# Kernel optimization log

Measured on AMD Instinct MI355X. Metric: run time of the kernel, lower is better.

## Reference

```python
import jax, jax.numpy as jnp
import numpy as np
import math


def setup_inputs() -> dict:
    key = jax.random.key(0)
    ks = jax.random.split(key, 10)
    b, n, d, h = 2, 1024, 1024, 16
    hd = d // h
    std = 0.02
    x = jax.random.normal(ks[0], (b, n, d), jnp.float32)
    Wq = jax.random.normal(ks[1], (d, d), jnp.float32) * std
    Wk = jax.random.normal(ks[2], (d, d), jnp.float32) * std
    Wv = jax.random.normal(ks[3], (d, d), jnp.float32) * std
    Wo = jax.random.normal(ks[4], (d, d), jnp.float32) * std
    Ww1 = jax.random.normal(ks[5], (d, hd), jnp.float32) * std
    Ww2 = jax.random.normal(ks[6], (hd, d), jnp.float32) * std
    Wb = jax.random.normal(ks[7], (d, h), jnp.float32) * std
    Wf = jax.random.normal(ks[8], (d, h), jnp.float32) * std
    # delta initialized so sigmoid(delta) = threshold = 0.99
    delta = jnp.full((h,), math.log(0.99 / (1.0 - 0.99)), jnp.float32)
    return dict(x=x, Wq=Wq, Wk=Wk, Wv=Wv, Wo=Wo, Ww1=Ww1, Ww2=Ww2, Wb=Wb, Wf=Wf, delta=delta)


def reference(x, Wq, Wk, Wv, Wo, Ww1, Ww2, Wb, Wf, delta):
    b, n, d = x.shape
    h = delta.shape[0]
    hd = d // h
    scale = hd ** -0.5
    q = (x @ Wq).reshape(b, n, h, hd)
    k = (x @ Wk).reshape(b, n, h, hd)
    v = (x @ Wv).reshape(b, n, h, hd)
    w = ((x @ Ww1) @ Ww2).reshape(b, n, h, hd)
    # l2-normalize write directions per head
    w = w * jax.lax.rsqrt(jnp.sum(w * w, axis=-1, keepdims=True) + 1e-6)
    beta = 2.0 * jax.nn.sigmoid(x @ Wb)                      # (b,n,h)
    log_f = jax.nn.log_sigmoid((x @ Wf + delta).astype(jnp.float32))  # (b,n,h)
    bt = jnp.transpose(beta, (0, 2, 1))                      # (b,h,n)
    # PaTH attention: logit_{t,j} = q_t^T H_t H_{t-1} ... H_{j+1} k_j, H_s = I - beta_s w_s w_s^T.
    # UT transform: c_{s,j} = w_s . k_j^{(s-1)} satisfies (I + L) C = tril(W K^T, -1)
    # with L_{s,r} = beta_r (w_s . w_r) for r < s.
    A = jnp.einsum('bshd,brhd->bhsr', w, w)                  # w_s . w_r
    L = jnp.tril(A, -1) * bt[:, :, None, :]                  # (b,h,n,n), strictly lower
    Mlow = jnp.tril(jnp.einsum('bshd,bjhd->bhsj', w, k), -1)
    C = jax.scipy.linalg.solve_triangular(L, Mlow, lower=True, unit_diagonal=True)
    # transformed score: S_{t,j} = q_t.k_j - sum_{j<s<=t} beta_s (q_t.w_s) c_{s,j}
    G = jnp.tril(jnp.einsum('bthd,bshd->bhts', q, w) * bt[:, :, None, :])
    S = jnp.einsum('bthd,bjhd->bhtj', q, k) - G @ C          # (b,h,n,n)
    # forgetting-gate decay: add F_t - F_j (cumulative log-sigmoid gates)
    Fc = jnp.cumsum(jnp.transpose(log_f, (0, 2, 1)), axis=-1)  # (b,h,n)
    logits = S * scale + Fc[..., :, None] - Fc[..., None, :]
    mask = jnp.tril(jnp.ones((n, n), bool))
    logits = jnp.where(mask, logits, -jnp.inf)
    P = jax.nn.softmax(logits, axis=-1)
    o = jnp.einsum('bhtj,bjhd->bthd', P, v).reshape(b, n, d)
    return o @ Wo
```

## Files before the change

### kernel.cpp

```cpp
#include <hip/hip_runtime.h>
#include <hip/hip_bf16.h>

#define DEV static __device__ __forceinline__

constexpr float SM_SCALE = 0.125f;

typedef __attribute__((ext_vector_type(8))) short s16x8;
typedef __attribute__((ext_vector_type(8))) unsigned short u16x8;
typedef __attribute__((ext_vector_type(4))) unsigned short u16x4;
typedef __attribute__((ext_vector_type(4))) float f32x4;

DEV float bf2f(unsigned short u) {
  union { unsigned int i; float f; } v; v.i = ((unsigned int)u) << 16; return v.f;
}
DEV unsigned short f2bf(float f) {
  union { float f; unsigned int i; } v; v.f = f;
  unsigned int r = v.i + 0x7fffu + ((v.i >> 16) & 1u);
  return (unsigned short)(r >> 16);
}
DEV void tri_unrank(int r, int& k, int& i) {
  k = (int)((sqrtf(8.f * r + 1.f) - 1.f) * 0.5f);
  while (k * (k + 1) / 2 > r) --k;
  while ((k + 1) * (k + 2) / 2 <= r) ++k;
  i = r - k * (k + 1) / 2;
}
DEV void glds16(const void* g, void* l) {
  __builtin_amdgcn_global_load_lds(
      (const __attribute__((address_space(1))) void*)g,
      (__attribute__((address_space(3))) void*)l, 16, 0, 0);
}

constexpr size_t OFF_XB   = 0;
constexpr size_t OFF_WQT  = 4194304;
constexpr size_t OFF_BL   = 4194304;
constexpr size_t OFF_WKT  = 6291456;
constexpr size_t OFF_BFT  = 6291456;
constexpr size_t OFF_WVT  = 8388608;
constexpr size_t OFF_WOT  = 10485760;
constexpr size_t OFF_W1T  = 12582912;
constexpr size_t OFF_W2T  = 12713984;
constexpr size_t OFF_Q16  = 12845056;
constexpr size_t OFF_K16  = 17039360;
constexpr size_t OFF_VT   = 21233664;
constexpr size_t OFF_WN16 = 25427968;
constexpr size_t OFF_WB16 = 29622272;
constexpr size_t OFF_WNF  = 33816576;
constexpr size_t OFF_OB   = 33816576;
constexpr size_t OFF_WPRE = 38010880;
constexpr size_t OFF_FC   = 38273024;
constexpr size_t OFF_L    = 38404096;
constexpr size_t OFF_CT   = 105512960;
constexpr size_t OFF_G    = 172621824;
constexpr size_t OFF_MR   = 239730688;
constexpr size_t OFF_LR   = 239861760;
constexpr size_t OFF_UI   = 239992832;
constexpr size_t OFF_U128 = 244187136;

__global__ __launch_bounds__(256) void prep_all(
    const float* __restrict__ W0, const float* __restrict__ W1,
    const float* __restrict__ W2, const float* __restrict__ W3,
    const float* __restrict__ Ww1, const float* __restrict__ Ww2,
    const float* __restrict__ x,
    unsigned short* __restrict__ D0, unsigned short* __restrict__ D1,
    unsigned short* __restrict__ D2, unsigned short* __restrict__ D3,
    unsigned short* __restrict__ D4, unsigned short* __restrict__ D5,
    unsigned short* __restrict__ xb) {
  int bidx = blockIdx.x;
  int t = threadIdx.x;
  if (bidx >= 1536) {
    int i = ((bidx - 1536) * 256 + t) * 8;
    float4 a = *(const float4*)(x + i);
    float4 b = *(const float4*)(x + i + 4);
    u16x8 o;
    o[0] = f2bf(a.x); o[1] = f2bf(a.y); o[2] = f2bf(a.z); o[3] = f2bf(a.w);
    o[4] = f2bf(b.x); o[5] = f2bf(b.y); o[6] = f2bf(b.z); o[7] = f2bf(b.w);
    *(u16x8*)(xb + i) = o;
    return;
  }
  int z = bidx >> 8, xy = bidx & 255;
  int bx = xy & 15, by = xy >> 4;
  const float* src; unsigned short* dst; int R, C;
  if (z == 0) { src = W0; dst = D0; R = 1024; C = 1024; }
  else if (z == 1) { src = W1; dst = D1; R = 1024; C = 1024; }
  else if (z == 2) { src = W2; dst = D2; R = 1024; C = 1024; }
  else if (z == 3) { src = W3; dst = D3; R = 1024; C = 1024; }
  else if (z == 4) { src = Ww1; dst = D4; R = 1024; C = 64; }
  else { src = Ww2; dst = D5; R = 64; C = 1024; }
  int c0 = bx * 64, r0 = by * 64;
  if (c0 >= C || r0 >= R) return;
  __shared__ float tile[64 * 65];
#pragma unroll
  for (int i = 0; i < 16; ++i) {
    int lin = t + i * 256; int r = lin >> 6, c = lin & 63;
    tile[r * 65 + c] = src[(size_t)(r0 + r) * C + c0 + c];
  }
  __syncthreads();
#pragma unroll
  for (int i = 0; i < 16; ++i) {
    int lin = t + i * 256; int c = lin >> 6, r = lin & 63;
    dst[(size_t)(c0 + c) * R + r0 + r] = f2bf(tile[r * 65 + c]);
  }
}

__global__ __launch_bounds__(256) void bfprep(const float* __restrict__ Wb,
    const float* __restrict__ Wf, unsigned short* __restrict__ BFT) {
  int idx = blockIdx.x * 256 + threadIdx.x;
  int j = idx >> 10, i = idx & 1023;
  float v = 0.f;
  if (j < 16) v = Wb[i * 16 + j];
  else if (j < 32) v = Wf[i * 16 + (j - 16)];
  BFT[idx] = f2bf(v);
}

__global__ __launch_bounds__(256) void bgfc(const float* __restrict__ BL,
    const float* __restrict__ delta, float* __restrict__ Beta, float* __restrict__ Fc) {
  int bh = blockIdx.x;
  int b = bh >> 4, h = bh & 15;
  int t = threadIdx.x;
  __shared__ float buf[1024];
  __shared__ float tsum[256];
  float dh = delta[h];
#pragma unroll
  for (int i = 0; i < 4; ++i) {
    int n = t + i * 256;
    int row = (b << 10) + n;
    float braw = BL[row * 64 + h];
    Beta[row * 16 + h] = 2.f / (1.f + __expf(-braw));
    float lraw = BL[row * 64 + 16 + h] + dh;
    buf[n] = (lraw >= 0.f) ? -log1pf(__expf(-lraw)) : (lraw - log1pf(__expf(lraw)));
  }
  __syncthreads();
  float loc[4]; float run = 0.f;
#pragma unroll
  for (int i = 0; i < 4; ++i) { run += buf[t * 4 + i]; loc[i] = run; }
  tsum[t] = run;
  __syncthreads();
  for (int off = 1; off < 256; off <<= 1) {
    float add = (t >= off) ? tsum[t - off] : 0.f;
    __syncthreads();
    tsum[t] += add;
    __syncthreads();
  }
  float excl = tsum[t] - run;
#pragma unroll
  for (int i = 0; i < 4; ++i) Fc[bh * 1024 + t * 4 + i] = excl + loc[i];
}

__global__ __launch_bounds__(256) void proj_big(const unsigned short* __restrict__ xb,
    const unsigned short* __restrict__ WqT, const unsigned short* __restrict__ WkT,
    const unsigned short* __restrict__ WvT, unsigned short* __restrict__ Q16,
    unsigned short* __restrict__ K16, unsigned short* __restrict__ VT) {
  int idx = blockIdx.x;
  const unsigned short *A, *BT; unsigned short* out; int m0, n0;
  if (idx < 256) {
    int my = idx >> 4, nx = idx & 15;
    m0 = my * 128; A = xb;
    if (nx < 8) { BT = WqT; out = Q16; n0 = nx * 128; }
    else { BT = WkT; out = K16; n0 = (nx - 8) * 128; }
  } else {
    int r = idx - 256; int bz = r >> 6; int rem = r & 63;
    m0 = (rem >> 3) * 128; n0 = (rem & 7) * 128;
    A = WvT; BT = xb + ((size_t)bz << 20); out = VT + ((size_t)bz << 20);
  }
  int t = threadIdx.x;
  int w = t >> 6, l = t & 63;
  int wr = w >> 1, wc = w & 1;
  int fr = l & 15, fq = l >> 4;
  __shared__ unsigned short As[128 * 64];
  __shared__ unsigned short Bs[128 * 64];
  f32x4 acc[4][4];
#pragma unroll
  for (int m = 0; m < 4; ++m)
#pragma unroll
    for (int c = 0; c < 4; ++c) acc[m][c] = (f32x4){0.f, 0.f, 0.f, 0.f};
  for (int k0 = 0; k0 < 1024; k0 += 64) {
    __syncthreads();
#pragma unroll
    for (int i = 0; i < 4; ++i) {
      int cid = t + i * 256;
      int row = cid >> 3, ch = cid & 7;
      int chs = ch ^ (row & 7);
      glds16(A + (size_t)(m0 + row) * 1024 + k0 + chs * 8, (char*)As + cid * 16);
      glds16(BT + (size_t)(n0 + row) * 1024 + k0 + chs * 8, (char*)Bs + cid * 16);
    }
    __syncthreads();
#pragma unroll
    for (int kh = 0; kh < 2; ++kh) {
      s16x8 af[4], bfv[4];
#pragma unroll
      for (int m = 0; m < 4; ++m) {
        int ra = wr * 64 + 16 * m + fr;
        af[m] = *(const s16x8*)((char*)As + (((ra << 7) + (kh << 6) + (fq << 4)) ^ ((ra & 7) << 4)));
      }
#pragma unroll
      for (int c = 0; c < 4; ++c) {
        int rb = wc * 64 + 16 * c + fr;
        bfv[c] = *(const s16x8*)((char*)Bs + (((rb << 7) + (kh << 6) + (fq << 4)) ^ ((rb & 7) << 4)));
      }
#pragma unroll
      for (int m = 0; m < 4; ++m)
#pragma unroll
        for (int c = 0; c < 4; ++c)
          acc[m][c] = __builtin_amdgcn_mfma_f32_16x16x32_bf16(af[m], bfv[c], acc[m][c], 0, 0, 0);
    }
  }
#pragma unroll
  for (int m = 0; m < 4; ++m) {
#pragma unroll
    for (int c = 0; c < 4; ++c) {
      int col = n0 + wc * 64 + 16 * c + fr;
#pragma unroll
      for (int r = 0; r < 4; ++r) {
        int grow = m0 + wr * 64 + 16 * m + fq * 4 + r;
        out[(size_t)grow * 1024 + col] = f2bf(acc[m][c][r]);
      }
    }
  }
}

__global__ __launch_bounds__(256) void proj_small(const unsigned short* __restrict__ A,
    const unsigned short* __restrict__ W1T, const unsigned short* __restrict__ BFT,
    unsigned short* __restrict__ Wpre, float* __restrict__ BL) {
  int nt = blockIdx.x;
  const unsigned short* BT = nt ? BFT : W1T;
  __shared__ unsigned short As[64 * 64];
  __shared__ unsigned short Bs[64 * 64];
  int m0 = blockIdx.y * 64;
  int t = threadIdx.x;
  int w = t >> 6, l = t & 63, fr = l & 15;
  int koB = (l >> 4) * 16;
  f32x4 acc[4];
#pragma unroll
  for (int c = 0; c < 4; ++c) acc[c] = (f32x4){0.f, 0.f, 0.f, 0.f};
  for (int k0 = 0; k0 < 1024; k0 += 64) {
    __syncthreads();
#pragma unroll
    for (int i = 0; i < 2; ++i) {
      int cid = t + i * 256;
      int row = cid >> 3, ch = cid & 7;
      int chs = ch ^ (row & 7);
      glds16(A + (size_t)(m0 + row) * 1024 + k0 + chs * 8, (char*)As + cid * 16);
      glds16(BT + (size_t)row * 1024 + k0 + chs * 8, (char*)Bs + cid * 16);
    }
    __syncthreads();
#pragma unroll
    for (int kh = 0; kh < 2; ++kh) {
      int ra = 16 * w + fr;
      s16x8 a = *(const s16x8*)((char*)As + (((ra << 7) + (kh << 6) + koB) ^ ((ra & 7) << 4)));
#pragma unroll
      for (int c = 0; c < 4; ++c) {
        int rb = 16 * c + fr;
        s16x8 bb = *(const s16x8*)((char*)Bs + (((rb << 7) + (kh << 6) + koB) ^ ((rb & 7) << 4)));
        acc[c] = __builtin_amdgcn_mfma_f32_16x16x32_bf16(a, bb, acc[c], 0, 0, 0);
      }
    }
  }
  int rbase = m0 + 16 * w + ((l >> 4) << 2);
#pragma unroll
  for (int c = 0; c < 4; ++c) {
    int col = 16 * c + fr;
#pragma unroll
    for (int r = 0; r < 4; ++r) {
      if (nt) BL[(size_t)(rbase + r) * 64 + col] = acc[c][r];
      else Wpre[(size_t)(rbase + r) * 64 + col] = f2bf(acc[c][r]);
    }
  }
}

template<int F32OUT>
__global__ __launch_bounds__(256) void gemm_nt(const unsigned short* __restrict__ A,
    const unsigned short* __restrict__ BT, void* __restrict__ out,
    int M, int N, int K) {
  __shared__ unsigned short As[64 * 64];
  __shared__ unsigned short Bs[64 * 64];
  int m0 = blockIdx.y * 64, n0 = blockIdx.x * 64;
  int t = threadIdx.x;
  int w = t >> 6, l = t & 63, fr = l & 15;
  int koB = (l >> 4) * 16;
  f32x4 acc[4];
#pragma unroll
  for (int c = 0; c < 4; ++c) acc[c] = (f32x4){0.f, 0.f, 0.f, 0.f};
  for (int k0 = 0; k0 < K; k0 += 64) {
    __syncthreads();
#pragma unroll
    for (int i = 0; i < 2; ++i) {
      int cid = t + i * 256;
      int row = cid >> 3, ch = cid & 7;
      int chs = ch ^ (row & 7);
      glds16(A + (size_t)(m0 + row) * K + k0 + chs * 8, (char*)As + cid * 16);
      glds16(BT + (size_t)(n0 + row) * K + k0 + chs * 8, (char*)Bs + cid * 16);
    }
    __syncthreads();
#pragma unroll
    for (int kh = 0; kh < 2; ++kh) {
      int ra = 16 * w + fr;
      s16x8 a = *(const s16x8*)((char*)As + (((ra << 7) + (kh << 6) + koB) ^ ((ra & 7) << 4)));
#pragma unroll
      for (int c = 0; c < 4; ++c) {
        int rb = 16 * c + fr;
        s16x8 bb = *(const s16x8*)((char*)Bs + (((rb << 7) + (kh << 6) + koB) ^ ((rb & 7) << 4)));
        acc[c] = __builtin_amdgcn_mfma_f32_16x16x32_bf16(a, bb, acc[c], 0, 0, 0);
      }
    }
  }
  int rbase = m0 + 16 * w + ((l >> 4) << 2);
#pragma unroll
  for (int c = 0; c < 4; ++c) {
    int col = n0 + 16 * c + fr;
#pragma unroll
    for (int r = 0; r < 4; ++r) {
      if (F32OUT) ((float*)out)[(size_t)(rbase + r) * N + col] = acc[c][r];
      else ((unsigned short*)out)[(size_t)(rbase + r) * N + col] = f2bf(acc[c][r]);
    }
  }
}

__global__ __launch_bounds__(256) void wnorm2(const unsigned short* __restrict__ WNF,
    const float* __restrict__ Beta, unsigned short* __restrict__ WN,
    unsigned short* __restrict__ WB) {
  int row = blockIdx.x;
  int wave = threadIdx.x >> 6, lane = threadIdx.x & 63;
#pragma unroll
  for (int i = 0; i < 4; ++i) {
    int hh = wave * 4 + i;
    size_t idx = ((size_t)row << 10) + hh * 64 + lane;
    float v = bf2f(WNF[idx]);
    float ss = v * v;
#pragma unroll
    for (int off = 1; off < 64; off <<= 1) ss += __shfl_xor(ss, off);
    float wn = v * rsqrtf(ss + 1e-6f);
    WN[idx] = f2bf(wn);
    WB[idx] = f2bf(wn * Beta[row * 16 + hh]);
  }
}

__global__ __launch_bounds__(256) void pairLG(const unsigned short* __restrict__ WN,
    const unsigned short* __restrict__ Q, const unsigned short* __restrict__ WB,
    unsigned short* __restrict__ Lg, unsigned short* __restrict__ Gg) {
  int idx = blockIdx.x;
  int bh = idx & 31, r0r = idx >> 5;
  int tb2, jb2; tri_unrank(r0r, tb2, jb2);
  int b = bh >> 4, h = bh & 15;
  int m0 = tb2 * 128, n0 = jb2 * 128;
  int t = threadIdx.x;
  int w = t >> 6, l = t & 63;
  int wr = w >> 1, wc = w & 1;
  int fr = l & 15, fq = l >> 4;
// ... 176 lines not shown
  }
}

__global__ __launch_bounds__(256) void u128build(const unsigned short* __restrict__ Lb,
    const unsigned short* __restrict__ UI, unsigned short* __restrict__ U128) {
  int ib = blockIdx.x, bh = blockIdx.y;
  int t = threadIdx.x, w = t >> 6, l = t & 63, fr = l & 15, fq = l >> 4;
  int s0 = ib * 128;
  size_t base = (size_t)bh << 20;
  const unsigned short* Ua = UI + (((size_t)(bh * 16 + 2 * ib)) << 12);
  const unsigned short* Uc = UI + (((size_t)(bh * 16 + 2 * ib + 1)) << 12);
  unsigned short* Uo = U128 + (((size_t)(bh * 8 + ib)) << 14);
  __shared__ unsigned short UaT[64 * 64];
  __shared__ unsigned short T1T[64 * 64];
#pragma unroll
  for (int i = 0; i < 2; ++i) {
    int cid = t + i * 256;
    int s = cid >> 3, ch = cid & 7;
    u16x8 v = *(const u16x8*)(Ua + s * 64 + ch * 8);
#pragma unroll
    for (int e = 0; e < 8; ++e) {
      int j = ch * 8 + e;
      int byt = ((j << 7) + (s << 1)) ^ ((j & 7) << 4);
      *(unsigned short*)((char*)UaT + byt) = v[e];
    }
  }
#pragma unroll
  for (int i = 0; i < 8; ++i) {
    int cid = t + i * 256;
    int row = cid >> 4, ch = cid & 15;
    if (row < 64) {
      if (ch < 8) *(u16x8*)(Uo + row * 128 + ch * 8) = *(const u16x8*)(Ua + row * 64 + ch * 8);
      else { u16x8 z = {0,0,0,0,0,0,0,0}; *(u16x8*)(Uo + row * 128 + ch * 8) = z; }
    } else if (ch >= 8) {
      *(u16x8*)(Uo + row * 128 + ch * 8) = *(const u16x8*)(Uc + (row - 64) * 64 + (ch - 8) * 8);
    }
  }
  __syncthreads();
  f32x4 a1[4];
#pragma unroll
  for (int c = 0; c < 4; ++c) a1[c] = (f32x4){0.f, 0.f, 0.f, 0.f};
#pragma unroll
  for (int kc = 0; kc < 2; ++kc) {
    s16x8 af = *(const s16x8*)(Lb + base + ((size_t)(s0 + 64 + 16 * w + fr) << 10) + s0 + kc * 32 + fq * 8);
#pragma unroll
    for (int c = 0; c < 4; ++c) {
      int j = 16 * c + fr;
      s16x8 bb = *(const s16x8*)((char*)UaT + (((j << 7) + (kc << 6) + (fq << 4)) ^ ((j & 7) << 4)));
      a1[c] = __builtin_amdgcn_mfma_f32_16x16x32_bf16(af, bb, a1[c], 0, 0, 0);
    }
  }
#pragma unroll
  for (int c = 0; c < 4; ++c) {
    int gj = 16 * c + fr;
    int sb = 16 * w + fq * 4;
    u16x4 pk;
#pragma unroll
    for (int r = 0; r < 4; ++r) pk[r] = f2bf(a1[c][r]);
    *(u16x4*)((char*)T1T + (((gj << 7) + (sb << 1)) ^ ((gj & 7) << 4))) = pk;
  }
  __syncthreads();
  f32x4 a2[4];
#pragma unroll
  for (int c = 0; c < 4; ++c) a2[c] = (f32x4){0.f, 0.f, 0.f, 0.f};
#pragma unroll
  for (int kc = 0; kc < 2; ++kc) {
    s16x8 af = *(const s16x8*)(Uc + (16 * w + fr) * 64 + kc * 32 + fq * 8);
#pragma unroll
    for (int c = 0; c < 4; ++c) {
      int j = 16 * c + fr;
      s16x8 bb = *(const s16x8*)((char*)T1T + (((j << 7) + (kc << 6) + (fq << 4)) ^ ((j & 7) << 4)));
      a2[c] = __builtin_amdgcn_mfma_f32_16x16x32_bf16(af, bb, a2[c], 0, 0, 0);
    }
  }
#pragma unroll
  for (int c = 0; c < 4; ++c) {
    int gj = 16 * c + fr;
#pragma unroll
    for (int r = 0; r < 4; ++r)
      Uo[(64 + 16 * w + fq * 4 + r) * 128 + gj] = f2bf(a2[c][r]);
  }
}

__global__ __launch_bounds__(256) void solve128(const unsigned short* __restrict__ WN,
    const unsigned short* __restrict__ Kk, const unsigned short* __restrict__ Lb,
    const unsigned short* __restrict__ U128, unsigned short* __restrict__ CT, int ib) {
  int jb = blockIdx.x, bh = blockIdx.y;
  int b = bh >> 4, h = bh & 15;
  int t = threadIdx.x, w = t >> 6, l = t & 63;
  int wr = w >> 1, wc = w & 1, fr = l & 15, fq = l >> 4;
  int s0 = ib * 128, j0 = jb * 128;
  size_t base = (size_t)bh << 20;
  __shared__ unsigned short sh[128 * 128];
  unsigned short* As = sh;
  unsigned short* Bs = sh + 128 * 64;
  unsigned short* rT = sh;
  const unsigned short* Wb_ = WN + ((size_t)b << 20) + h * 64;
  const unsigned short* Kb_ = Kk + ((size_t)b << 20) + h * 64;

  f32x4 acc[4][4];
#pragma unroll
  for (int m = 0; m < 4; ++m)
#pragma unroll
    for (int c = 0; c < 4; ++c) acc[m][c] = (f32x4){0.f, 0.f, 0.f, 0.f};
  int nst = (jb == ib) ? 1 : 1 + 2 * (ib - jb);
  for (int st = 0; st < nst; ++st) {
    __syncthreads();
#pragma unroll
    for (int i = 0; i < 4; ++i) {
      int cid = t + i * 256;
      int row = cid >> 3, ch = cid & 7;
      int chs = ch ^ (row & 7);
      const unsigned short *ga, *gb;
      if (st == 0) {
        ga = Wb_ + ((size_t)(s0 + row) << 10) + chs * 8;
        gb = Kb_ + ((size_t)(j0 + row) << 10) + chs * 8;
      } else {
        int rb = 2 * jb + st - 1;
        ga = Lb + base + ((size_t)(s0 + row) << 10) + rb * 64 + chs * 8;
        gb = CT + base + ((size_t)(j0 + row) << 10) + rb * 64 + chs * 8;
      }
      glds16(ga, (char*)As + cid * 16);
      glds16(gb, (char*)Bs + cid * 16);
    }
    __syncthreads();
#pragma unroll
    for (int kh = 0; kh < 2; ++kh) {
      s16x8 af[4], bfv[4];
#pragma unroll
      for (int m = 0; m < 4; ++m) {
        int ra = wr * 64 + 16 * m + fr;
        af[m] = *(const s16x8*)((char*)As + (((ra << 7) + (kh << 6) + (fq << 4)) ^ ((ra & 7) << 4)));
      }
#pragma unroll
      for (int c = 0; c < 4; ++c) {
        int rb2 = wc * 64 + 16 * c + fr;
        bfv[c] = *(const s16x8*)((char*)Bs + (((rb2 << 7) + (kh << 6) + (fq << 4)) ^ ((rb2 & 7) << 4)));
      }
#pragma unroll
      for (int m = 0; m < 4; ++m)
#pragma unroll
        for (int c = 0; c < 4; ++c)
          acc[m][c] = __builtin_amdgcn_mfma_f32_16x16x32_bf16(af[m], bfv[c], acc[m][c], 0, 0, 0);
    }
  }
  __syncthreads();
#pragma unroll
  for (int m = 0; m < 4; ++m) {
#pragma unroll
    for (int c = 0; c < 4; ++c) {
      int jl = wc * 64 + 16 * c + fr;
      int sb = wr * 64 + 16 * m + fq * 4;
      u16x4 pk;
#pragma unroll
      for (int r = 0; r < 4; ++r) {
        float v = acc[m][c][r];
        if (jb == ib && jl >= sb + r) v = 0.f;
        pk[r] = f2bf(v);
      }
      int byt = ((jl << 8) + (sb << 1)) ^ ((jl & 15) << 4);
      *(u16x4*)((char*)rT + byt) = pk;
    }
  }
  __syncthreads();
  const unsigned short* U = U128 + (((size_t)(bh * 8 + ib)) << 14);
  f32x4 a2[4][4];
#pragma unroll
  for (int m = 0; m < 4; ++m)
#pragma unroll
    for (int c = 0; c < 4; ++c) a2[m][c] = (f32x4){0.f, 0.f, 0.f, 0.f};
#pragma unroll
  for (int kc = 0; kc < 4; ++kc) {
    s16x8 uf[4], bfv[4];
#pragma unroll
    for (int m = 0; m < 4; ++m)
      uf[m] = *(const s16x8*)(U + (wr * 64 + 16 * m + fr) * 128 + kc * 32 + fq * 8);
#pragma unroll
    for (int c = 0; c < 4; ++c) {
      int jl = wc * 64 + 16 * c + fr;
      bfv[c] = *(const s16x8*)((char*)rT + (((jl << 8) + (kc << 6) + (fq << 4)) ^ ((jl & 15) << 4)));
    }
#pragma unroll
    for (int m = 0; m < 4; ++m)
#pragma unroll
      for (int c = 0; c < 4; ++c)
        a2[m][c] = __builtin_amdgcn_mfma_f32_16x16x32_bf16(uf[m], bfv[c], a2[m][c], 0, 0, 0);
  }
#pragma unroll
  for (int m = 0; m < 4; ++m) {
#pragma unroll
    for (int c = 0; c < 4; ++c) {
      int gj = wc * 64 + 16 * c + fr;
      int sb = wr * 64 + 16 * m + fq * 4;
      u16x4 pk;
#pragma unroll
      for (int r = 0; r < 4; ++r) pk[r] = f2bf(a2[m][c][r]);
      *(u16x4*)(CT + base + ((size_t)(j0 + gj) << 10) + s0 + sb) = pk;
    }
  }
}

__global__ __launch_bounds__(256) void rowstat(const unsigned short* __restrict__ S,
    const float* __restrict__ Fc, float* __restrict__ MR, float* __restrict__ LR) {
  int bh = blockIdx.y;
  int t = blockIdx.x * 4 + (threadIdx.x >> 6);
  int l = threadIdx.x & 63;
  size_t base = (size_t)bh << 20;
  const unsigned short* srow = S + base + ((size_t)t << 10);
  float vals[16]; float vmax = -1e30f;
#pragma unroll
  for (int i = 0; i < 2; ++i) {
    int c0 = i * 512 + l * 8;
    u16x8 sv = *(const u16x8*)(srow + c0);
    float4 f0 = *(const float4*)(Fc + bh * 1024 + c0);
    float4 f1 = *(const float4*)(Fc + bh * 1024 + c0 + 4);
#pragma unroll
    for (int e = 0; e < 8; ++e) {
      float fc = e < 4 ? ((const float*)&f0)[e] : ((const float*)&f1)[e - 4];
      float v = (c0 + e <= t) ? bf2f(sv[e]) * SM_SCALE - fc : -1e30f;
      vals[i * 8 + e] = v; vmax = fmaxf(vmax, v);
    }
  }
#pragma unroll
  for (int o = 1; o < 64; o <<= 1) vmax = fmaxf(vmax, __shfl_xor(vmax, o));
  float sum = 0.f;
#pragma unroll
  for (int e = 0; e < 16; ++e) sum += __expf(vals[e] - vmax);
#pragma unroll
  for (int o = 1; o < 64; o <<= 1) sum += __shfl_xor(sum, o);
  if (l == 0) { MR[bh * 1024 + t] = vmax; LR[bh * 1024 + t] = sum; }
}

__global__ __launch_bounds__(256) void pv_kernel(const unsigned short* __restrict__ S,
    const unsigned short* __restrict__ VT, const float* __restrict__ Fc,
    const float* __restrict__ MR, const float* __restrict__ LR,
    unsigned short* __restrict__ Ob) {
  int idx = blockIdx.x;
  int bh = idx & 31, rank = idx >> 5;
  int tb = 15 - rank;
  int b = bh >> 4, h = bh & 15;
  int t0 = tb * 64;
  int t = threadIdx.x, w = t >> 6, l = t & 63, fr = l & 15, fq = l >> 4;
  __shared__ unsigned short Pl[64 * 64];
  size_t base = (size_t)bh << 20;
  f32x4 acc[4];
#pragma unroll
  for (int c = 0; c < 4; ++c) acc[c] = (f32x4){0.f,0.f,0.f,0.f};
  for (int jb = 0; jb <= tb; ++jb) {
    int j0 = jb * 64;
    __syncthreads();
#pragma unroll
    for (int i = 0; i < 2; ++i) {
      int cid = t + i * 256;
      int row = cid >> 3, ch = cid & 7;
      int grow = t0 + row;
      u16x8 sv = *(const u16x8*)(S + base + ((size_t)grow << 10) + j0 + ch * 8);
      float4 f0 = *(const float4*)(Fc + bh * 1024 + j0 + ch * 8);
      float4 f1 = *(const float4*)(Fc + bh * 1024 + j0 + ch * 8 + 4);
      float m = MR[bh * 1024 + grow];
      u16x8 pv;
#pragma unroll
      for (int e = 0; e < 8; ++e) {
        float fc = e < 4 ? ((const float*)&f0)[e] : ((const float*)&f1)[e - 4];
        float p = __expf(bf2f(sv[e]) * SM_SCALE - fc - m);
        if (jb == tb && ch * 8 + e > row) p = 0.f;
        pv[e] = f2bf(p);
      }
      int byt = ((row << 7) + (ch << 4)) ^ ((row & 7) << 4);
      *(u16x8*)((char*)Pl + byt) = pv;
    }
    __syncthreads();
#pragma unroll
    for (int kh = 0; kh < 2; ++kh) {
      int ra = 16 * w + fr;
      s16x8 a = *(const s16x8*)((char*)Pl + (((ra << 7) + (kh << 6) + (fq << 4)) ^ ((ra & 7) << 4)));
#pragma unroll
      for (int c = 0; c < 4; ++c) {
        s16x8 bb = *(const s16x8*)(VT + ((size_t)bh * 64 + 16 * c + fr) * 1024 + j0 + kh * 32 + fq * 8);
        acc[c] = __builtin_amdgcn_mfma_f32_16x16x32_bf16(a, bb, acc[c], 0, 0, 0);
      }
    }
  }
  float inv[4];
#pragma unroll
  for (int r = 0; r < 4; ++r) inv[r] = 1.f / LR[bh * 1024 + t0 + 16 * w + fq * 4 + r];
#pragma unroll
  for (int c = 0; c < 4; ++c) {
#pragma unroll
    for (int r = 0; r < 4; ++r) {
      int grow = t0 + 16 * w + fq * 4 + r;
      Ob[((size_t)(b * 1024) + grow) * 1024 + h * 64 + 16 * c + fr] = f2bf(acc[c][r] * inv[r]);
    }
  }
}

extern "C" void kernel_launch(void* const* d_in, const int* in_sizes, int n_in,
                              void* d_out, int out_size, void* d_ws, size_t ws_size,
                              hipStream_t stream) {
  const float* x    = (const float*)d_in[0];
  const float* Wq   = (const float*)d_in[1];
  const float* Wk   = (const float*)d_in[2];
  const float* Wv   = (const float*)d_in[3];
  const float* Wo   = (const float*)d_in[4];
  const float* Ww1  = (const float*)d_in[5];
  const float* Ww2  = (const float*)d_in[6];
  const float* Wb   = (const float*)d_in[7];
  const float* Wf   = (const float*)d_in[8];
  const float* delta= (const float*)d_in[9];

  char* ws = (char*)d_ws;
  unsigned short* xb   = (unsigned short*)(ws + OFF_XB);
  unsigned short* WqT  = (unsigned short*)(ws + OFF_WQT);
  float*          BL   = (float*)(ws + OFF_BL);
  unsigned short* WkT  = (unsigned short*)(ws + OFF_WKT);
  unsigned short* BFT  = (unsigned short*)(ws + OFF_BFT);
  unsigned short* WvT  = (unsigned short*)(ws + OFF_WVT);
  unsigned short* WoT  = (unsigned short*)(ws + OFF_WOT);
  unsigned short* W1T  = (unsigned short*)(ws + OFF_W1T);
  unsigned short* W2T  = (unsigned short*)(ws + OFF_W2T);
  float*          Beta = (float*)(ws + OFF_W1T);
  unsigned short* Q16  = (unsigned short*)(ws + OFF_Q16);
  unsigned short* K16  = (unsigned short*)(ws + OFF_K16);
  unsigned short* VT   = (unsigned short*)(ws + OFF_VT);
  unsigned short* WN16 = (unsigned short*)(ws + OFF_WN16);
  unsigned short* WB16 = (unsigned short*)(ws + OFF_WB16);
  unsigned short* WNF16= (unsigned short*)(ws + OFF_WNF);
  unsigned short* ObB  = (unsigned short*)(ws + OFF_OB);
  unsigned short* Wpre = (unsigned short*)(ws + OFF_WPRE);
  float*          Fc   = (float*)(ws + OFF_FC);
  unsigned short* Lbuf = (unsigned short*)(ws + OFF_L);
  unsigned short* Sbuf = (unsigned short*)(ws + OFF_L);
  unsigned short* CT   = (unsigned short*)(ws + OFF_CT);
  unsigned short* Gbuf = (unsigned short*)(ws + OFF_G);
  float*          MR   = (float*)(ws + OFF_MR);
  float*          LR   = (float*)(ws + OFF_LR);
  unsigned short* UI   = (unsigned short*)(ws + OFF_UI);
  unsigned short* U128 = (unsigned short*)(ws + OFF_U128);

  dim3 blk(256);
  prep_all<<<2560, blk, 0, stream>>>(Wq, Wk, Wv, Wo, Ww1, Ww2, x,
                                     WqT, WkT, WvT, WoT, W1T, W2T, xb);
  proj_big<<<384, blk, 0, stream>>>(xb, WqT, WkT, WvT, Q16, K16, VT);
  bfprep<<<256, blk, 0, stream>>>(Wb, Wf, BFT);
  proj_small<<<dim3(2,32), blk, 0, stream>>>(xb, W1T, BFT, Wpre, BL);
  gemm_nt<0><<<dim3(16,32), blk, 0, stream>>>(Wpre, W2T, WNF16, 2048, 1024, 64);
  bgfc<<<32, blk, 0, stream>>>(BL, delta, Beta, Fc);
  wnorm2<<<2048, blk, 0, stream>>>(WNF16, Beta, WN16, WB16);
  pairLG<<<dim3(36 * 32), blk, 0, stream>>>(WN16, Q16, WB16, Lbuf, Gbuf);
  inv64<<<dim3(16,32), blk, 0, stream>>>(Lbuf, UI);
  u128build<<<dim3(8,32), blk, 0, stream>>>(Lbuf, UI, U128);
  for (int ib = 0; ib < 8; ++ib)
    solve128<<<dim3(ib + 1, 32), blk, 0, stream>>>(WN16, K16, Lbuf, U128, CT, ib);
  score128s<<<dim3(36 * 32), blk, 0, stream>>>(Q16, K16, Gbuf, CT, Sbuf);
  rowstat<<<dim3(256,32), blk, 0, stream>>>(Sbuf, Fc, MR, LR);
  pv_kernel<<<dim3(512), blk, 0, stream>>>(Sbuf, VT, Fc, MR, LR, ObB);
  gemm_nt<1><<<dim3(16,32), blk, 0, stream>>>(ObB, WoT, d_out, 2048, 1024, 1024);
}
```

Measured before the change: 337.5 us.

## Use 256-row blocked triangular solve and fold Ww1·Ww2 into a single projection weight

The blocked forward-substitution solve now uses 256-row diagonal blocks instead of 128. A new kernel builds the inverse of each 256 block from pairs of 128 inverses, so the sequential solve needs 4 launches instead of 8 and each block does more MFMA work. The low-rank write projection is reassociated: Ww1·Ww2 is precomputed as one 1024x1024 weight and added to the main projection GEMM, and the Wb/Wf prep is merged into the prep kernel. This removes launches and serial dependency depth, at the cost of extra FLOPs for the dense w projection and bf16 rounding of the combined weight.

```diff
diff --git a/kernel.cpp b/kernel.cpp
--- a/kernel.cpp
+++ b/kernel.cpp
@@ -34,11 +34,11 @@
 constexpr size_t OFF_WQT  = 4194304;
 constexpr size_t OFF_BL   = 4194304;
 constexpr size_t OFF_WKT  = 6291456;
-constexpr size_t OFF_BFT  = 6291456;
 constexpr size_t OFF_WVT  = 8388608;
 constexpr size_t OFF_WOT  = 10485760;
-constexpr size_t OFF_W1T  = 12582912;
+constexpr size_t OFF_W1C  = 12582912;
 constexpr size_t OFF_W2T  = 12713984;
+constexpr size_t OFF_BETA = 12582912;
 constexpr size_t OFF_Q16  = 12845056;
 constexpr size_t OFF_K16  = 17039360;
 constexpr size_t OFF_VT   = 21233664;
@@ -46,7 +46,7 @@
 constexpr size_t OFF_WB16 = 29622272;
 constexpr size_t OFF_WNF  = 33816576;
 constexpr size_t OFF_OB   = 33816576;
-constexpr size_t OFF_WPRE = 38010880;
+constexpr size_t OFF_BFT  = 38010880;
 constexpr size_t OFF_FC   = 38273024;
 constexpr size_t OFF_L    = 38404096;
 constexpr size_t OFF_CT   = 105512960;
@@ -55,20 +55,47 @@
 constexpr size_t OFF_LR   = 239861760;
 constexpr size_t OFF_UI   = 239992832;
 constexpr size_t OFF_U128 = 244187136;
+constexpr size_t OFF_B256 = 252575744;
 
 __global__ __launch_bounds__(256) void prep_all(
     const float* __restrict__ W0, const float* __restrict__ W1,
     const float* __restrict__ W2, const float* __restrict__ W3,
     const float* __restrict__ Ww1, const float* __restrict__ Ww2,
-    const float* __restrict__ x,
+    const float* __restrict__ x, const float* __restrict__ Wb,
+    const float* __restrict__ Wf,
     unsigned short* __restrict__ D0, unsigned short* __restrict__ D1,
     unsigned short* __restrict__ D2, unsigned short* __restrict__ D3,
-    unsigned short* __restrict__ D4, unsigned short* __restrict__ D5,
-    unsigned short* __restrict__ xb) {
+    unsigned short* __restrict__ W1c, unsigned short* __restrict__ W2T,
+    unsigned short* __restrict__ xb, unsigned short* __restrict__ BFT) {
   int bidx = blockIdx.x;
   int t = threadIdx.x;
-  if (bidx >= 1536) {
-    int i = ((bidx - 1536) * 256 + t) * 8;
+  if (bidx >= 2096) {
+    int e0 = ((bidx - 2096) * 256 + t) * 8;
+    int j = e0 >> 10, i0 = e0 & 1023;
+    u16x8 o;
+#pragma unroll
+    for (int e = 0; e < 8; ++e) {
+      int i = i0 + e;
+      float v = 0.f;
+      if (j < 16) v = Wb[i * 16 + j];
+      else if (j < 32) v = Wf[i * 16 + (j - 16)];
+      o[e] = f2bf(v);
+    }
+    *(u16x8*)(BFT + e0) = o;
+    return;
+  }
+  if (bidx >= 2064) {
+    int i = ((bidx - 2064) * 256 + t) * 8;
+    float4 a = *(const float4*)(Ww1 + i);
+    float4 b = *(const float4*)(Ww1 + i + 4);
+    u16x8 o;
+    o[0] = f2bf(a.x); o[1] = f2bf(a.y); o[2] = f2bf(a.z); o[3] = f2bf(a.w);
+    o[4] = f2bf(b.x); o[5] = f2bf(b.y); o[6] = f2bf(b.z); o[7] = f2bf(b.w);
+    *(u16x8*)(W1c + i) = o;
+    return;
+  }
+  if (bidx >= 1040) {
+    int i = ((bidx - 1040) * 256 + t) * 8;
     float4 a = *(const float4*)(x + i);
     float4 b = *(const float4*)(x + i + 4);
     u16x8 o;
@@ -77,17 +104,17 @@
     *(u16x8*)(xb + i) = o;
     return;
   }
-  int z = bidx >> 8, xy = bidx & 255;
-  int bx = xy & 15, by = xy >> 4;
-  const float* src; unsigned short* dst; int R, C;
-  if (z == 0) { src = W0; dst = D0; R = 1024; C = 1024; }
-  else if (z == 1) { src = W1; dst = D1; R = 1024; C = 1024; }
-  else if (z == 2) { src = W2; dst = D2; R = 1024; C = 1024; }
-  else if (z == 3) { src = W3; dst = D3; R = 1024; C = 1024; }
-  else if (z == 4) { src = Ww1; dst = D4; R = 1024; C = 64; }
-  else { src = Ww2; dst = D5; R = 64; C = 1024; }
-  int c0 = bx * 64, r0 = by * 64;
-  if (c0 >= C || r0 >= R) return;
+  const float* src; unsigned short* dst; int R, C, c0, r0;
+  if (bidx >= 1024) {
+    src = Ww2; dst = W2T; R = 64; C = 1024;
+    c0 = (bidx - 1024) * 64; r0 = 0;
+  } else {
+    int z = bidx >> 8, xy = bidx & 255;
+    src = z == 0 ? W0 : z == 1 ? W1 : z == 2 ? W2 : W3;
+    dst = z == 0 ? D0 : z == 1 ? D1 : z == 2 ? D2 : D3;
+    R = 1024; C = 1024;
+    c0 = (xy & 15) * 64; r0 = (xy >> 4) * 64;
+  }
   __shared__ float tile[64 * 65];
 #pragma unroll
   for (int i = 0; i < 16; ++i) {
@@ -100,16 +127,6 @@
     int lin = t + i * 256; int c = lin >> 6, r = lin & 63;
     dst[(size_t)(c0 + c) * R + r0 + r] = f2bf(tile[r * 65 + c]);
   }
-}
-
-__global__ __launch_bounds__(256) void bfprep(const float* __restrict__ Wb,
-    const float* __restrict__ Wf, unsigned short* __restrict__ BFT) {
-  int idx = blockIdx.x * 256 + threadIdx.x;
-  int j = idx >> 10, i = idx & 1023;
-  float v = 0.f;
-  if (j < 16) v = Wb[i * 16 + j];
-  else if (j < 32) v = Wf[i * 16 + (j - 16)];
-  BFT[idx] = f2bf(v);
 }
 
 __global__ __launch_bounds__(256) void bgfc(const float* __restrict__ BL,
@@ -148,8 +165,9 @@
 
 __global__ __launch_bounds__(256) void proj_big(const unsigned short* __restrict__ xb,
     const unsigned short* __restrict__ WqT, const unsigned short* __restrict__ WkT,
-    const unsigned short* __restrict__ WvT, unsigned short* __restrict__ Q16,
-    unsigned short* __restrict__ K16, unsigned short* __restrict__ VT) {
+    const unsigned short* __restrict__ WvT, const unsigned short* __restrict__ WfT,
+    unsigned short* __restrict__ Q16, unsigned short* __restrict__ K16,
+    unsigned short* __restrict__ VT, unsigned short* __restrict__ WNF) {
   int idx = blockIdx.x;
   const unsigned short *A, *BT; unsigned short* out; int m0, n0;
   if (idx < 256) {
@@ -157,10 +175,14 @@
     m0 = my * 128; A = xb;
     if (nx < 8) { BT = WqT; out = Q16; n0 = nx * 128; }
     else { BT = WkT; out = K16; n0 = (nx - 8) * 128; }
-  } else {
+  } else if (idx < 384) {
     int r = idx - 256; int bz = r >> 6; int rem = r & 63;
     m0 = (rem >> 3) * 128; n0 = (rem & 7) * 128;
     A = WvT; BT = xb + ((size_t)bz << 20); out = VT + ((size_t)bz << 20);
+  } else {
+    int r2 = idx - 384;
+    m0 = (r2 >> 3) * 128; n0 = (r2 & 7) * 128;
+    A = xb; BT = WfT; out = WNF;
   }
   int t = threadIdx.x;
   int w = t >> 6, l = t & 63;
@@ -214,55 +236,6 @@
         int grow = m0 + wr * 64 + 16 * m + fq * 4 + r;
         out[(size_t)grow * 1024 + col] = f2bf(acc[m][c][r]);
       }
-    }
-  }
-}
-
-__global__ __launch_bounds__(256) void proj_small(const unsigned short* __restrict__ A,
-    const unsigned short* __restrict__ W1T, const unsigned short* __restrict__ BFT,
-    unsigned short* __restrict__ Wpre, float* __restrict__ BL) {
-  int nt = blockIdx.x;
-  const unsigned short* BT = nt ? BFT : W1T;
-  __shared__ unsigned short As[64 * 64];
-  __shared__ unsigned short Bs[64 * 64];
-  int m0 = blockIdx.y * 64;
-  int t = threadIdx.x;
-  int w = t >> 6, l = t & 63, fr = l & 15;
-  int koB = (l >> 4) * 16;
-  f32x4 acc[4];
-#pragma unroll
-  for (int c = 0; c < 4; ++c) acc[c] = (f32x4){0.f, 0.f, 0.f, 0.f};
-  for (int k0 = 0; k0 < 1024; k0 += 64) {
-    __syncthreads();
-#pragma unroll
-    for (int i = 0; i < 2; ++i) {
-      int cid = t + i * 256;
-      int row = cid >> 3, ch = cid & 7;
-      int chs = ch ^ (row & 7);
-      glds16(A + (size_t)(m0 + row) * 1024 + k0 + chs * 8, (char*)As + cid * 16);
-      glds16(BT + (size_t)row * 1024 + k0 + chs * 8, (char*)Bs + cid * 16);
-    }
-    __syncthreads();
-#pragma unroll
-    for (int kh = 0; kh < 2; ++kh) {
-      int ra = 16 * w + fr;
-      s16x8 a = *(const s16x8*)((char*)As + (((ra << 7) + (kh << 6) + koB) ^ ((ra & 7) << 4)));
-#pragma unroll
-      for (int c = 0; c < 4; ++c) {
-        int rb = 16 * c + fr;
-        s16x8 bb = *(const s16x8*)((char*)Bs + (((rb << 7) + (kh << 6) + koB) ^ ((rb & 7) << 4)));
-        acc[c] = __builtin_amdgcn_mfma_f32_16x16x32_bf16(a, bb, acc[c], 0, 0, 0);
-      }
-    }
-  }
-  int rbase = m0 + 16 * w + ((l >> 4) << 2);
-#pragma unroll
-  for (int c = 0; c < 4; ++c) {
-    int col = 16 * c + fr;
-#pragma unroll
-    for (int r = 0; r < 4; ++r) {
-      if (nt) BL[(size_t)(rbase + r) * 64 + col] = acc[c][r];
-      else Wpre[(size_t)(rbase + r) * 64 + col] = f2bf(acc[c][r]);
     }
   }
 }
@@ -605,65 +578,159 @@
   }
 }
 
-__global__ __launch_bounds__(256) void solve128(const unsigned short* __restrict__ WN,
+__global__ __launch_bounds__(256) void u256build(const unsigned short* __restrict__ Lb,
+    const unsigned short* __restrict__ U128, unsigned short* __restrict__ B256) {
+  int qb = blockIdx.x, bh = blockIdx.y;
+  int t = threadIdx.x, w = t >> 6, l = t & 63, fr = l & 15, fq = l >> 4;
+  int s0 = qb * 256;
+  size_t base = (size_t)bh << 20;
+  const unsigned short* Ua = U128 + (((size_t)(bh * 8 + 2 * qb)) << 14);
+  const unsigned short* Uc = U128 + (((size_t)(bh * 8 + 2 * qb + 1)) << 14);
+  unsigned short* out = B256 + (((size_t)(bh * 4 + qb)) << 14);
+  __shared__ unsigned short UaT[16384];
+  __shared__ unsigned short T1T[16384];
+#pragma unroll
+  for (int i = 0; i < 8; ++i) {
+    int cid = t + i * 256;
+    int s = cid >> 4, ch = cid & 15;
+    u16x8 v = *(const u16x8*)(Ua + s * 128 + ch * 8);
+#pragma unroll
+    for (int e = 0; e < 8; ++e) {
+      int j = ch * 8 + e;
+      int byt = ((j << 8) + (s << 1)) ^ ((j & 15) << 4);
+      *(unsigned short*)((char*)UaT + byt) = v[e];
+    }
+  }
+  __syncthreads();
+  f32x4 a1[2][8];
+#pragma unroll
+  for (int m = 0; m < 2; ++m)
+#pragma unroll
+    for (int c = 0; c < 8; ++c) a1[m][c] = (f32x4){0.f, 0.f, 0.f, 0.f};
+#pragma unroll
+  for (int kc = 0; kc < 4; ++kc) {
+    s16x8 af[2];
+#pragma unroll
+    for (int m = 0; m < 2; ++m)
+      af[m] = *(const s16x8*)(Lb + base + ((size_t)(s0 + 128 + 32 * w + 16 * m + fr) << 10) + s0 + kc * 32 + fq * 8);
+#pragma unroll
+    for (int c = 0; c < 8; ++c) {
+      int j = 16 * c + fr;
+      s16x8 bb = *(const s16x8*)((char*)UaT + (((j << 8) + (kc << 6) + (fq << 4)) ^ ((j & 15) << 4)));
+#pragma unroll
+      for (int m = 0; m < 2; ++m)
+        a1[m][c] = __builtin_amdgcn_mfma_f32_16x16x32_bf16(af[m], bb, a1[m][c], 0, 0, 0);
+    }
+  }
+#pragma unroll
+  for (int m = 0; m < 2; ++m) {
+#pragma unroll
+    for (int c = 0; c < 8; ++c) {
+      int col = 16 * c + fr;
+      int row0 = 32 * w + 16 * m + fq * 4;
+      u16x4 pk;
+#pragma unroll
+      for (int r = 0; r < 4; ++r) pk[r] = f2bf(a1[m][c][r]);
+      int byt = ((col << 8) + (row0 << 1)) ^ ((col & 15) << 4);
+      *(u16x4*)((char*)T1T + byt) = pk;
+    }
+  }
+  __syncthreads();
+  f32x4 a2[2][8];
+#pragma unroll
+  for (int m = 0; m < 2; ++m)
+#pragma unroll
+    for (int c = 0; c < 8; ++c) a2[m][c] = (f32x4){0.f, 0.f, 0.f, 0.f};
+#pragma unroll
+  for (int kc = 0; kc < 4; ++kc) {
+    s16x8 af[2];
+#pragma unroll
+    for (int m = 0; m < 2; ++m)
+      af[m] = *(const s16x8*)(Uc + (32 * w + 16 * m + fr) * 128 + kc * 32 + fq * 8);
+#pragma unroll
+    for (int c = 0; c < 8; ++c) {
+      int j = 16 * c + fr;
+      s16x8 bb = *(const s16x8*)((char*)T1T + (((j << 8) + (kc << 6) + (fq << 4)) ^ ((j & 15) << 4)));
+#pragma unroll
+      for (int m = 0; m < 2; ++m)
+        a2[m][c] = __builtin_amdgcn_mfma_f32_16x16x32_bf16(af[m], bb, a2[m][c], 0, 0, 0);
+    }
+  }
+#pragma unroll
+  for (int m = 0; m < 2; ++m) {
+#pragma unroll
+    for (int c = 0; c < 8; ++c) {
+      int col = 16 * c + fr;
+#pragma unroll
+      for (int r = 0; r < 4; ++r)
+        out[(32 * w + 16 * m + fq * 4 + r) * 128 + col] = f2bf(a2[m][c][r]);
+    }
+  }
+}
+
+__global__ __launch_bounds__(256) void solve256(const unsigned short* __restrict__ WN,
     const unsigned short* __restrict__ Kk, const unsigned short* __restrict__ Lb,
-    const unsigned short* __restrict__ U128, unsigned short* __restrict__ CT, int ib) {
+    const unsigned short* __restrict__ U128, const unsigned short* __restrict__ B256,
+    unsigned short* __restrict__ CT, int ib) {
   int jb = blockIdx.x, bh = blockIdx.y;
   int b = bh >> 4, h = bh & 15;
-  int t = threadIdx.x, w = t >> 6, l = t & 63;
-  int wr = w >> 1, wc = w & 1, fr = l & 15, fq = l >> 4;
-  int s0 = ib * 128, j0 = jb * 128;
+  int t = threadIdx.x, w = t >> 6, l = t & 63, fr = l & 15, fq = l >> 4;
+  int s0 = ib * 256, j0 = jb * 128;
   size_t base = (size_t)bh << 20;
-  __shared__ unsigned short sh[128 * 128];
+  __shared__ unsigned short sh[32768];
   unsigned short* As = sh;
-  unsigned short* Bs = sh + 128 * 64;
+  unsigned short* Bs = sh + 16384;
   unsigned short* rT = sh;
   const unsigned short* Wb_ = WN + ((size_t)b << 20) + h * 64;
   const unsigned short* Kb_ = Kk + ((size_t)b << 20) + h * 64;
 
-  f32x4 acc[4][4];
+  f32x4 acc[4][8];
 #pragma unroll
   for (int m = 0; m < 4; ++m)
 #pragma unroll
-    for (int c = 0; c < 4; ++c) acc[m][c] = (f32x4){0.f, 0.f, 0.f, 0.f};
-  int nst = (jb == ib) ? 1 : 1 + 2 * (ib - jb);
+    for (int c = 0; c < 8; ++c) acc[m][c] = (f32x4){0.f, 0.f, 0.f, 0.f};
+  int nst = 1 + 4 * ib - 2 * jb; if (nst < 1) nst = 1;
   for (int st = 0; st < nst; ++st) {
     __syncthreads();
+    int rb = 2 * jb + st - 1;
+#pragma unroll
+    for (int i = 0; i < 8; ++i) {
+      int cid = t + i * 256;
+      int row = cid >> 3, ch = cid & 7;
+      int chs = ch ^ (row & 7);
+      const unsigned short* ga = (st == 0)
+        ? Wb_ + ((size_t)(s0 + row) << 10) + chs * 8
+        : Lb + base + ((size_t)(s0 + row) << 10) + rb * 64 + chs * 8;
+      glds16(ga, (char*)As + cid * 16);
+    }
 #pragma unroll
     for (int i = 0; i < 4; ++i) {
       int cid = t + i * 256;
       int row = cid >> 3, ch = cid & 7;
       int chs = ch ^ (row & 7);
-      const unsigned short *ga, *gb;
-      if (st == 0) {
-        ga = Wb_ + ((size_t)(s0 + row) << 10) + chs * 8;
-        gb = Kb_ + ((size_t)(j0 + row) << 10) + chs * 8;
-      } else {
-        int rb = 2 * jb + st - 1;
-        ga = Lb + base + ((size_t)(s0 + row) << 10) + rb * 64 + chs * 8;
-        gb = CT + base + ((size_t)(j0 + row) << 10) + rb * 64 + chs * 8;
-      }
-      glds16(ga, (char*)As + cid * 16);
+      const unsigned short* gb = (st == 0)
+        ? Kb_ + ((size_t)(j0 + row) << 10) + chs * 8
+        : CT + base + ((size_t)(j0 + row) << 10) + rb * 64 + chs * 8;
       glds16(gb, (char*)Bs + cid * 16);
     }
     __syncthreads();
 #pragma unroll
     for (int kh = 0; kh < 2; ++kh) {
-      s16x8 af[4], bfv[4];
+      s16x8 af[4], bfv[8];
 #pragma unroll
       for (int m = 0; m < 4; ++m) {
-        int ra = wr * 64 + 16 * m + fr;
+        int ra = 64 * w + 16 * m + fr;
         af[m] = *(const s16x8*)((char*)As + (((ra << 7) + (kh << 6) + (fq << 4)) ^ ((ra & 7) << 4)));
       }
 #pragma unroll
-      for (int c = 0; c < 4; ++c) {
-        int rb2 = wc * 64 + 16 * c + fr;
+      for (int c = 0; c < 8; ++c) {
+        int rb2 = 16 * c + fr;
         bfv[c] = *(const s16x8*)((char*)Bs + (((rb2 << 7) + (kh << 6) + (fq << 4)) ^ ((rb2 & 7) << 4)));
       }
 #pragma unroll
       for (int m = 0; m < 4; ++m)
 #pragma unroll
-        for (int c = 0; c < 4; ++c)
+        for (int c = 0; c < 8; ++c)
           acc[m][c] = __builtin_amdgcn_mfma_f32_16x16x32_bf16(af[m], bfv[c], acc[m][c], 0, 0, 0);
     }
   }
@@ -671,54 +738,56 @@
 #pragma unroll
   for (int m = 0; m < 4; ++m) {
 #pragma unroll
-    for (int c = 0; c < 4; ++c) {
-      int jl = wc * 64 + 16 * c + fr;
-      int sb = wr * 64 + 16 * m + fq * 4;
+    for (int c = 0; c < 8; ++c) {
+      int sl0 = 64 * w + 16 * m + fq * 4;
+      int jl = 16 * c + fr;
       u16x4 pk;
 #pragma unroll
       for (int r = 0; r < 4; ++r) {
         float v = acc[m][c][r];
-        if (jb == ib && jl >= sb + r) v = 0.f;
+        if (j0 + jl >= s0 + sl0 + r) v = 0.f;
         pk[r] = f2bf(v);
       }
-      int byt = ((jl << 8) + (sb << 1)) ^ ((jl & 15) << 4);
+      int byt = ((jl << 9) + (sl0 << 1)) ^ ((jl & 15) << 4);
       *(u16x4*)((char*)rT + byt) = pk;
     }
   }
   __syncthreads();
-  const unsigned short* U = U128 + (((size_t)(bh * 8 + ib)) << 14);
-  f32x4 a2[4][4];
+  const unsigned short* Ua = U128 + (((size_t)(bh * 8 + 2 * ib)) << 14);
+  const unsigned short* Uc = U128 + (((size_t)(bh * 8 + 2 * ib + 1)) << 14);
+  const unsigned short* Bm = B256 + (((size_t)(bh * 4 + ib)) << 14);
 #pragma unroll
   for (int m = 0; m < 4; ++m)
 #pragma unroll
-    for (int c = 0; c < 4; ++c) a2[m][c] = (f32x4){0.f, 0.f, 0.f, 0.f};
-#pragma unroll
-  for (int kc = 0; kc < 4; ++kc) {
-    s16x8 uf[4], bfv[4];
+    for (int c = 0; c < 8; ++c) acc[m][c] = (f32x4){0.f, 0.f, 0.f, 0.f};
+  int nkc = (w < 2) ? 4 : 8;
+  for (int kc = 0; kc < nkc; ++kc) {
+    const unsigned short* src; int arow;
+    if (w < 2) { src = Ua; arow = 64 * w; }
+    else { src = (kc < 4) ? Bm : Uc; arow = 64 * (w - 2); }
+    s16x8 uf[4];
 #pragma unroll
     for (int m = 0; m < 4; ++m)
-      uf[m] = *(const s16x8*)(U + (wr * 64 + 16 * m + fr) * 128 + kc * 32 + fq * 8);
-#pragma unroll
-    for (int c = 0; c < 4; ++c) {
-      int jl = wc * 64 + 16 * c + fr;
-      bfv[c] = *(const s16x8*)((char*)rT + (((jl << 8) + (kc << 6) + (fq << 4)) ^ ((jl & 15) << 4)));
-    }
-#pragma unroll
-    for (int m = 0; m < 4; ++m)
-#pragma unroll
-      for (int c = 0; c < 4; ++c)
-        a2[m][c] = __builtin_amdgcn_mfma_f32_16x16x32_bf16(uf[m], bfv[c], a2[m][c], 0, 0, 0);
+      uf[m] = *(const s16x8*)(src + (arow + 16 * m + fr) * 128 + (kc & 3) * 32 + fq * 8);
+#pragma unroll
+    for (int c = 0; c < 8; ++c) {
+      int jl = 16 * c + fr;
+      s16x8 bb = *(const s16x8*)((char*)rT + (((jl << 9) + (kc << 6) + (fq << 4)) ^ ((jl & 15) << 4)));
+#pragma unroll
+      for (int m = 0; m < 4; ++m)
+        acc[m][c] = __builtin_amdgcn_mfma_f32_16x16x32_bf16(uf[m], bb, acc[m][c], 0, 0, 0);
+    }
   }
 #pragma unroll
   for (int m = 0; m < 4; ++m) {
 #pragma unroll
-    for (int c = 0; c < 4; ++c) {
-      int gj = wc * 64 + 16 * c + fr;
-      int sb = wr * 64 + 16 * m + fq * 4;
+    for (int c = 0; c < 8; ++c) {
+      int jl = 16 * c + fr;
+      int sb = 64 * w + 16 * m + fq * 4;
       u16x4 pk;
 #pragma unroll
-      for (int r = 0; r < 4; ++r) pk[r] = f2bf(a2[m][c][r]);
-      *(u16x4*)(CT + base + ((size_t)(j0 + gj) << 10) + s0 + sb) = pk;
+      for (int r = 0; r < 4; ++r) pk[r] = f2bf(acc[m][c][r]);
+      *(u16x4*)(CT + base + ((size_t)(j0 + jl) << 10) + s0 + sb) = pk;
     }
   }
 }
@@ -836,12 +905,11 @@
   unsigned short* WqT  = (unsigned short*)(ws + OFF_WQT);
   float*          BL   = (float*)(ws + OFF_BL);
   unsigned short* WkT  = (unsigned short*)(ws + OFF_WKT);
-  unsigned short* BFT  = (unsigned short*)(ws + OFF_BFT);
   unsigned short* WvT  = (unsigned short*)(ws + OFF_WVT);
   unsigned short* WoT  = (unsigned short*)(ws + OFF_WOT);
-  unsigned short* W1T  = (unsigned short*)(ws + OFF_W1T);
+  unsigned short* W1c  = (unsigned short*)(ws + OFF_W1C);
   unsigned short* W2T  = (unsigned short*)(ws + OFF_W2T);
-  float*          Beta = (float*)(ws + OFF_W1T);
+  float*          Beta = (float*)(ws + OFF_BETA);
   unsigned short* Q16  = (unsigned short*)(ws + OFF_Q16);
   unsigned short* K16  = (unsigned short*)(ws + OFF_K16);
   unsigned short* VT   = (unsigned short*)(ws + OFF_VT);
@@ -849,7 +917,7 @@
   unsigned short* WB16 = (unsigned short*)(ws + OFF_WB16);
   unsigned short* WNF16= (unsigned short*)(ws + OFF_WNF);
   unsigned short* ObB  = (unsigned short*)(ws + OFF_OB);
-  unsigned short* Wpre = (unsigned short*)(ws + OFF_WPRE);
+  unsigned short* BFT  = (unsigned short*)(ws + OFF_BFT);
   float*          Fc   = (float*)(ws + OFF_FC);
   unsigned short* Lbuf = (unsigned short*)(ws + OFF_L);
   unsigned short* Sbuf = (unsigned short*)(ws + OFF_L);
@@ -859,21 +927,22 @@
   float*          LR   = (float*)(ws + OFF_LR);
   unsigned short* UI   = (unsigned short*)(ws + OFF_UI);
   unsigned short* U128 = (unsigned short*)(ws + OFF_U128);
+  unsigned short* B256 = (unsigned short*)(ws + OFF_B256);
 
   dim3 blk(256);
-  prep_all<<<2560, blk, 0, stream>>>(Wq, Wk, Wv, Wo, Ww1, Ww2, x,
-                                     WqT, WkT, WvT, WoT, W1T, W2T, xb);
-  proj_big<<<384, blk, 0, stream>>>(xb, WqT, WkT, WvT, Q16, K16, VT);
-  bfprep<<<256, blk, 0, stream>>>(Wb, Wf, BFT);
-  proj_small<<<dim3(2,32), blk, 0, stream>>>(xb, W1T, BFT, Wpre, BL);
-  gemm_nt<0><<<dim3(16,32), blk, 0, stream>>>(Wpre, W2T, WNF16, 2048, 1024, 64);
+  prep_all<<<2128, blk, 0, stream>>>(Wq, Wk, Wv, Wo, Ww1, Ww2, x, Wb, Wf,
+                                     WqT, WkT, WvT, WoT, W1c, W2T, xb, BFT);
+  gemm_nt<0><<<dim3(16,16), blk, 0, stream>>>(W2T, W1c, WN16, 1024, 1024, 64);
+  proj_big<<<512, blk, 0, stream>>>(xb, WqT, WkT, WvT, WN16, Q16, K16, VT, WNF16);
+  gemm_nt<1><<<dim3(1,32), blk, 0, stream>>>(xb, BFT, BL, 2048, 64, 1024);
   bgfc<<<32, blk, 0, stream>>>(BL, delta, Beta, Fc);
   wnorm2<<<2048, blk, 0, stream>>>(WNF16, Beta, WN16, WB16);
   pairLG<<<dim3(36 * 32), blk, 0, stream>>>(WN16, Q16, WB16, Lbuf, Gbuf);
   inv64<<<dim3(16,32), blk, 0, stream>>>(Lbuf, UI);
   u128build<<<dim3(8,32), blk, 0, stream>>>(Lbuf, UI, U128);
-  for (int ib = 0; ib < 8; ++ib)
-    solve128<<<dim3(ib + 1, 32), blk, 0, stream>>>(WN16, K16, Lbuf, U128, CT, ib);
+  u256build<<<dim3(4,32), blk, 0, stream>>>(Lbuf, U128, B256);
+  for (int ib = 0; ib < 4; ++ib)
+    solve256<<<dim3(2 * ib + 2, 32), blk, 0, stream>>>(WN16, K16, Lbuf, U128, B256, CT, ib);
   score128s<<<dim3(36 * 32), blk, 0, stream>>>(Q16, K16, Gbuf, CT, Sbuf);
   rowstat<<<dim3(256,32), blk, 0, stream>>>(Sbuf, Fc, MR, LR);
   pv_kernel<<<dim3(512), blk, 0, stream>>>(Sbuf, VT, Fc, MR, LR, ObB);
```

Measured after the change: 316.1 us. -6.3%, faster.
